# Performance work log

Measured on AMD Instinct MI355X. Metric: run time of the kernel, lower is better.

## Reference

```python
import jax, jax.numpy as jnp
import numpy as np

LN_EPS = 1e-5
LEAKY_SLOPE = 0.01


def setup_inputs() -> dict:
    key = jax.random.key(0)
    k1, k2, k3 = jax.random.split(key, 3)
    n, d, ns = 200000, 512, 1024
    x = jax.random.normal(k1, (n, d), dtype=jnp.float32)
    # Kaiming-ish scale for the projection weight [3d, d]
    W = jax.random.normal(k2, (3 * d, d), dtype=jnp.float32) * (1.0 / np.sqrt(3 * d))
    b = jnp.zeros((d,), dtype=jnp.float32)
    gamma = jnp.ones((d,), dtype=jnp.float32)
    beta = jnp.zeros((d,), dtype=jnp.float32)
    batch = jnp.sort(jax.random.randint(k3, (n,), 0, ns, dtype=jnp.int32))
    return {"x": x, "W": W, "b": b, "gamma": gamma, "beta": beta,
            "batch": batch, "num_segments": ns}


def _pool_mean_max_std(x, batch, num_segments):
    # single-pass style segment reductions: sum, sum-of-squares, count, max
    n = x.shape[0]
    count = jax.ops.segment_sum(jnp.ones((n,), x.dtype), batch, num_segments)  # [S]
    s = jax.ops.segment_sum(x, batch, num_segments)                            # [S,d]
    sq = jax.ops.segment_sum(x * x, batch, num_segments)                       # [S,d]
    cnt = jnp.maximum(count, 1.0)[:, None]
    mean = s / cnt                                                             # global_mean_pool
    # masked dense amax == segment max; empty segments -> finfo.min (NEG fill)
    NEG = jnp.finfo(x.dtype).min
    xmax = jax.ops.segment_max(x, batch, num_segments)
    xmax = jnp.where(jnp.isfinite(xmax), xmax, NEG)
    # scatter_std, unbiased=True, divisor clamped to >= 1 (torch_scatter semantics)
    var = (sq - mean * s) / jnp.maximum(count - 1.0, 1.0)[:, None]
    var = jnp.maximum(var, 0.0)
    safe = jnp.where(var > 0, var, 1.0)
    std = jnp.where(var > 0, jnp.sqrt(safe), 0.0)
    return jnp.concatenate([mean, xmax, std], axis=-1)  # [S, 3d]


def reference(x, W, b, gamma, beta, batch, num_segments):
    pooled = _pool_mean_max_std(x, batch, num_segments)        # [S, 3d]
    h = pooled @ W + b                                          # Linear
    mu = jnp.mean(h, axis=-1, keepdims=True)                    # LayerNorm (eps=1e-5)
    v = jnp.mean((h - mu) ** 2, axis=-1, keepdims=True)
    h = (h - mu) / jnp.sqrt(v + LN_EPS) * gamma + beta
    return jnp.where(h >= 0, h, LEAKY_SLOPE * h)                # LeakyReLU
```

## Files before the change

### kernel.cpp

```cpp
#include <hip/hip_runtime.h>
#include <math.h>

#define D 512
#define K3D 1536
#define NEGF (-3.40282346638528859812e+38f)

__device__ __forceinline__ int lower_bound_dev(const int* __restrict__ b, int n, int v) {
    int lo = 0, hi = n;
    while (lo < hi) {
        int mid = (lo + hi) >> 1;
        if (b[mid] < v) lo = mid + 1; else hi = mid;
    }
    return lo;
}

__device__ __forceinline__ void acc4(float4& s, float4& q, float4& m, const float4 v) {
    s.x += v.x; s.y += v.y; s.z += v.z; s.w += v.w;
    q.x = fmaf(v.x, v.x, q.x); q.y = fmaf(v.y, v.y, q.y);
    q.z = fmaf(v.z, v.z, q.z); q.w = fmaf(v.w, v.w, q.w);
    m.x = fmaxf(m.x, v.x); m.y = fmaxf(m.y, v.y);
    m.z = fmaxf(m.z, v.z); m.w = fmaxf(m.w, v.w);
}

__global__ __launch_bounds__(128) void pool_kernel(
    const float* __restrict__ x, const int* __restrict__ batch,
    float* __restrict__ pooled, int n) {
    const int s = blockIdx.x;
    const int tid = threadIdx.x;
    const int start = lower_bound_dev(batch, n, s);
    const int end   = lower_bound_dev(batch, n, s + 1);

    const float4* __restrict__ xv = (const float4*)x;

    float4 sum = {0.f, 0.f, 0.f, 0.f};
    float4 sq  = {0.f, 0.f, 0.f, 0.f};
    float4 mx  = {-INFINITY, -INFINITY, -INFINITY, -INFINITY};

    int i = start;
    for (; i + 4 <= end; i += 4) {
        float4 v0 = xv[(size_t)(i + 0) * 128 + tid];
        float4 v1 = xv[(size_t)(i + 1) * 128 + tid];
        float4 v2 = xv[(size_t)(i + 2) * 128 + tid];
        float4 v3 = xv[(size_t)(i + 3) * 128 + tid];
        acc4(sum, sq, mx, v0);
        acc4(sum, sq, mx, v1);
        acc4(sum, sq, mx, v2);
        acc4(sum, sq, mx, v3);
    }
    for (; i < end; ++i) {
        float4 v0 = xv[(size_t)i * 128 + tid];
        acc4(sum, sq, mx, v0);
    }

    const float cnt  = (float)(end - start);
    const float inv  = 1.f / fmaxf(cnt, 1.f);
    const float dinv = 1.f / fmaxf(cnt - 1.f, 1.f);

    float4 mean, stdv, mxo;
    mean.x = sum.x * inv; mean.y = sum.y * inv; mean.z = sum.z * inv; mean.w = sum.w * inv;

    float vx = (sq.x - mean.x * sum.x) * dinv;
    float vy = (sq.y - mean.y * sum.y) * dinv;
    float vz = (sq.z - mean.z * sum.z) * dinv;
    float vw = (sq.w - mean.w * sum.w) * dinv;
    vx = fmaxf(vx, 0.f); vy = fmaxf(vy, 0.f); vz = fmaxf(vz, 0.f); vw = fmaxf(vw, 0.f);
    stdv.x = vx > 0.f ? sqrtf(vx) : 0.f;
    stdv.y = vy > 0.f ? sqrtf(vy) : 0.f;
    stdv.z = vz > 0.f ? sqrtf(vz) : 0.f;
    stdv.w = vw > 0.f ? sqrtf(vw) : 0.f;

    mxo.x = isfinite(mx.x) ? mx.x : NEGF;
    mxo.y = isfinite(mx.y) ? mx.y : NEGF;
    mxo.z = isfinite(mx.z) ? mx.z : NEGF;
    mxo.w = isfinite(mx.w) ? mx.w : NEGF;

    float4* prow = (float4*)(pooled + (size_t)s * K3D);
    prow[tid]       = mean;
    prow[128 + tid] = mxo;
    prow[256 + tid] = stdv;
}

#define BM 32
#define BN 64
#define BK 32
#define LDA 36

__global__ __launch_bounds__(128) void gemm_kernel(
    const float* __restrict__ A, const float* __restrict__ W,
    const float* __restrict__ bias, float* __restrict__ H) {
    __shared__ __align__(16) float AsT[BK * LDA];
    __shared__ __align__(16) float Bs[BK * BN];

    const int tid = threadIdx.x;
    const int m0 = blockIdx.y * BM;
    const int j0 = blockIdx.x * BN;
    const int tr = tid >> 4;
    const int tc = tid & 15;

    const int kq = tid & 7;
    const int am = tid >> 3;
    const int jq = tid & 15;
    const int kr = tid >> 4;

    float acc[4][4] = {};

    for (int k0 = 0; k0 < K3D; k0 += BK) {
        float4 a0 = *(const float4*)&A[(size_t)(m0 + am)      * K3D + k0 + 4 * kq];
        float4 a1 = *(const float4*)&A[(size_t)(m0 + am + 16) * K3D + k0 + 4 * kq];
        float4 b0 = *(const float4*)&W[(size_t)(k0 + kr)      * D + j0 + 4 * jq];
        float4 b1 = *(const float4*)&W[(size_t)(k0 + kr +  8) * D + j0 + 4 * jq];
        float4 b2 = *(const float4*)&W[(size_t)(k0 + kr + 16) * D + j0 + 4 * jq];
        float4 b3 = *(const float4*)&W[(size_t)(k0 + kr + 24) * D + j0 + 4 * jq];

        __syncthreads();
        AsT[(4 * kq + 0) * LDA + am] = a0.x;
        AsT[(4 * kq + 1) * LDA + am] = a0.y;
        AsT[(4 * kq + 2) * LDA + am] = a0.z;
        AsT[(4 * kq + 3) * LDA + am] = a0.w;
        AsT[(4 * kq + 0) * LDA + am + 16] = a1.x;
        AsT[(4 * kq + 1) * LDA + am + 16] = a1.y;
        AsT[(4 * kq + 2) * LDA + am + 16] = a1.z;
        AsT[(4 * kq + 3) * LDA + am + 16] = a1.w;
        *(float4*)&Bs[(kr)      * BN + 4 * jq] = b0;
        *(float4*)&Bs[(kr +  8) * BN + 4 * jq] = b1;
        *(float4*)&Bs[(kr + 16) * BN + 4 * jq] = b2;
        *(float4*)&Bs[(kr + 24) * BN + 4 * jq] = b3;
        __syncthreads();

#pragma unroll
        for (int kk = 0; kk < BK; ++kk) {
            float4 av = *(const float4*)&AsT[kk * LDA + 4 * tr];
            float4 bv = *(const float4*)&Bs[kk * BN + 4 * tc];
            acc[0][0] = fmaf(av.x, bv.x, acc[0][0]);
            acc[0][1] = fmaf(av.x, bv.y, acc[0][1]);
            acc[0][2] = fmaf(av.x, bv.z, acc[0][2]);
            acc[0][3] = fmaf(av.x, bv.w, acc[0][3]);
            acc[1][0] = fmaf(av.y, bv.x, acc[1][0]);
            acc[1][1] = fmaf(av.y, bv.y, acc[1][1]);
            acc[1][2] = fmaf(av.y, bv.z, acc[1][2]);
            acc[1][3] = fmaf(av.y, bv.w, acc[1][3]);
            acc[2][0] = fmaf(av.z, bv.x, acc[2][0]);
            acc[2][1] = fmaf(av.z, bv.y, acc[2][1]);
            acc[2][2] = fmaf(av.z, bv.z, acc[2][2]);
            acc[2][3] = fmaf(av.z, bv.w, acc[2][3]);
            acc[3][0] = fmaf(av.w, bv.x, acc[3][0]);
            acc[3][1] = fmaf(av.w, bv.y, acc[3][1]);
            acc[3][2] = fmaf(av.w, bv.z, acc[3][2]);
            acc[3][3] = fmaf(av.w, bv.w, acc[3][3]);
        }
    }

    const float4 bb = *(const float4*)&bias[j0 + 4 * tc];
#pragma unroll
    for (int i = 0; i < 4; ++i) {
        float4 o;
        o.x = acc[i][0] + bb.x;
        o.y = acc[i][1] + bb.y;
        o.z = acc[i][2] + bb.z;
        o.w = acc[i][3] + bb.w;
        *(float4*)&H[(size_t)(m0 + 4 * tr + i) * D + j0 + 4 * tc] = o;
    }
}

__global__ __launch_bounds__(128) void ln_kernel(
    const float* __restrict__ H, const float* __restrict__ gamma,
    const float* __restrict__ beta, float* __restrict__ out) {
    const int row = blockIdx.x;
    const int tid = threadIdx.x;
    float4 v = *(const float4*)&H[(size_t)row * D + 4 * tid];

    float s = v.x + v.y + v.z + v.w;
    float q = v.x * v.x + v.y * v.y + v.z * v.z + v.w * v.w;
#pragma unroll
    for (int off = 32; off > 0; off >>= 1) {
        s += __shfl_down(s, off);
        q += __shfl_down(q, off);
    }
    __shared__ float ls[2], lq[2];
    const int wave = tid >> 6, lane = tid & 63;
    if (lane == 0) { ls[wave] = s; lq[wave] = q; }
    __syncthreads();
    s = ls[0] + ls[1];
    q = lq[0] + lq[1];

    const float mu = s * (1.f / 512.f);
    float var = q * (1.f / 512.f) - mu * mu;
    var = fmaxf(var, 0.f);
    const float r = rsqrtf(var + 1e-5f);

    float4 g  = *(const float4*)&gamma[4 * tid];
    float4 bt = *(const float4*)&beta[4 * tid];
    float4 o;
    o.x = (v.x - mu) * r * g.x + bt.x;
    o.y = (v.y - mu) * r * g.y + bt.y;
    o.z = (v.z - mu) * r * g.z + bt.z;
    o.w = (v.w - mu) * r * g.w + bt.w;
    o.x = o.x >= 0.f ? o.x : 0.01f * o.x;
    o.y = o.y >= 0.f ? o.y : 0.01f * o.y;
    o.z = o.z >= 0.f ? o.z : 0.01f * o.z;
    o.w = o.w >= 0.f ? o.w : 0.01f * o.w;
    *(float4*)&out[(size_t)row * D + 4 * tid] = o;
}

extern "C" void kernel_launch(void* const* d_in, const int* in_sizes, int n_in,
                              void* d_out, int out_size, void* d_ws, size_t ws_size,
                              hipStream_t stream) {
    const float* x     = (const float*)d_in[0];
    const float* W     = (const float*)d_in[1];
    const float* b     = (const float*)d_in[2];
    const float* gamma = (const float*)d_in[3];
    const float* beta  = (const float*)d_in[4];
    const int*   batch = (const int*)d_in[5];
    const int n = in_sizes[5];
    const int S = out_size / D;

    float* pooled = (float*)d_ws;
    float* H      = pooled + (size_t)S * K3D;
    float* out    = (float*)d_out;

    pool_kernel<<<S, 128, 0, stream>>>(x, batch, pooled, n);
    dim3 g2(D / BN, S / BM);
    gemm_kernel<<<g2, 128, 0, stream>>>(pooled, W, b, H);
    ln_kernel<<<S, 128, 0, stream>>>(H, gamma, beta, out);
}
```

Baseline: 625.2 us.

## Use two row-groups per pool block and split-K GEMM with reduction in LayerNorm

The pool kernel now runs 256 threads per segment, with two row-interleaved groups whose partial sum, sum-of-squares and max are combined through shared memory. The GEMM is split along K into four chunks, which multiplies the grid from 256 blocks to 1024 and fills more of the GPU. Each chunk writes its own partial output, and the LayerNorm kernel adds the four partials plus the bias. This costs extra workspace, more global traffic for the partials, and a small change in floating-point summation order.

```diff
diff --git a/kernel.cpp b/kernel.cpp
--- a/kernel.cpp
+++ b/kernel.cpp
@@ -22,11 +22,12 @@
     m.z = fmaxf(m.z, v.z); m.w = fmaxf(m.w, v.w);
 }
 
-__global__ __launch_bounds__(128) void pool_kernel(
+__global__ __launch_bounds__(256) void pool_kernel(
     const float* __restrict__ x, const int* __restrict__ batch,
     float* __restrict__ pooled, int n) {
-    const int s = blockIdx.x;
-    const int tid = threadIdx.x;
+    const int s   = blockIdx.x;
+    const int col = threadIdx.x & 127;
+    const int rw  = threadIdx.x >> 7;
     const int start = lower_bound_dev(batch, n, s);
     const int end   = lower_bound_dev(batch, n, s + 1);
 
@@ -36,64 +37,84 @@
     float4 sq  = {0.f, 0.f, 0.f, 0.f};
     float4 mx  = {-INFINITY, -INFINITY, -INFINITY, -INFINITY};
 
-    int i = start;
-    for (; i + 4 <= end; i += 4) {
-        float4 v0 = xv[(size_t)(i + 0) * 128 + tid];
-        float4 v1 = xv[(size_t)(i + 1) * 128 + tid];
-        float4 v2 = xv[(size_t)(i + 2) * 128 + tid];
-        float4 v3 = xv[(size_t)(i + 3) * 128 + tid];
+    int i = start + rw;
+    for (; i + 6 < end; i += 8) {
+        float4 v0 = xv[(size_t)(i + 0) * 128 + col];
+        float4 v1 = xv[(size_t)(i + 2) * 128 + col];
+        float4 v2 = xv[(size_t)(i + 4) * 128 + col];
+        float4 v3 = xv[(size_t)(i + 6) * 128 + col];
         acc4(sum, sq, mx, v0);
         acc4(sum, sq, mx, v1);
         acc4(sum, sq, mx, v2);
         acc4(sum, sq, mx, v3);
     }
-    for (; i < end; ++i) {
-        float4 v0 = xv[(size_t)i * 128 + tid];
+    for (; i < end; i += 2) {
+        float4 v0 = xv[(size_t)i * 128 + col];
         acc4(sum, sq, mx, v0);
     }
 
-    const float cnt  = (float)(end - start);
-    const float inv  = 1.f / fmaxf(cnt, 1.f);
-    const float dinv = 1.f / fmaxf(cnt - 1.f, 1.f);
-
-    float4 mean, stdv, mxo;
-    mean.x = sum.x * inv; mean.y = sum.y * inv; mean.z = sum.z * inv; mean.w = sum.w * inv;
-
-    float vx = (sq.x - mean.x * sum.x) * dinv;
-    float vy = (sq.y - mean.y * sum.y) * dinv;
-    float vz = (sq.z - mean.z * sum.z) * dinv;
-    float vw = (sq.w - mean.w * sum.w) * dinv;
-    vx = fmaxf(vx, 0.f); vy = fmaxf(vy, 0.f); vz = fmaxf(vz, 0.f); vw = fmaxf(vw, 0.f);
-    stdv.x = vx > 0.f ? sqrtf(vx) : 0.f;
-    stdv.y = vy > 0.f ? sqrtf(vy) : 0.f;
-    stdv.z = vz > 0.f ? sqrtf(vz) : 0.f;
-    stdv.w = vw > 0.f ? sqrtf(vw) : 0.f;
-
-    mxo.x = isfinite(mx.x) ? mx.x : NEGF;
-    mxo.y = isfinite(mx.y) ? mx.y : NEGF;
-    mxo.z = isfinite(mx.z) ? mx.z : NEGF;
-    mxo.w = isfinite(mx.w) ? mx.w : NEGF;
-
-    float4* prow = (float4*)(pooled + (size_t)s * K3D);
-    prow[tid]       = mean;
-    prow[128 + tid] = mxo;
-    prow[256 + tid] = stdv;
+    __shared__ __align__(16) float4 red[3 * 128];
+    if (rw == 1) {
+        red[col]       = sum;
+        red[128 + col] = sq;
+        red[256 + col] = mx;
+    }
+    __syncthreads();
+    if (rw == 0) {
+        float4 s2 = red[col], q2 = red[128 + col], m2 = red[256 + col];
+        sum.x += s2.x; sum.y += s2.y; sum.z += s2.z; sum.w += s2.w;
+        sq.x  += q2.x; sq.y  += q2.y; sq.z  += q2.z; sq.w  += q2.w;
+        mx.x = fmaxf(mx.x, m2.x); mx.y = fmaxf(mx.y, m2.y);
+        mx.z = fmaxf(mx.z, m2.z); mx.w = fmaxf(mx.w, m2.w);
+
+        const float cnt  = (float)(end - start);
+        const float inv  = 1.f / fmaxf(cnt, 1.f);
+        const float dinv = 1.f / fmaxf(cnt - 1.f, 1.f);
+
+        float4 mean, stdv, mxo;
+        mean.x = sum.x * inv; mean.y = sum.y * inv;
+        mean.z = sum.z * inv; mean.w = sum.w * inv;
+
+        float vx = (sq.x - mean.x * sum.x) * dinv;
+        float vy = (sq.y - mean.y * sum.y) * dinv;
+        float vz = (sq.z - mean.z * sum.z) * dinv;
+        float vw = (sq.w - mean.w * sum.w) * dinv;
+        vx = fmaxf(vx, 0.f); vy = fmaxf(vy, 0.f);
+        vz = fmaxf(vz, 0.f); vw = fmaxf(vw, 0.f);
+        stdv.x = vx > 0.f ? sqrtf(vx) : 0.f;
+        stdv.y = vy > 0.f ? sqrtf(vy) : 0.f;
+        stdv.z = vz > 0.f ? sqrtf(vz) : 0.f;
+        stdv.w = vw > 0.f ? sqrtf(vw) : 0.f;
+
+        mxo.x = isfinite(mx.x) ? mx.x : NEGF;
+        mxo.y = isfinite(mx.y) ? mx.y : NEGF;
+        mxo.z = isfinite(mx.z) ? mx.z : NEGF;
+        mxo.w = isfinite(mx.w) ? mx.w : NEGF;
+
+        float4* prow = (float4*)(pooled + (size_t)s * K3D);
+        prow[col]       = mean;
+        prow[128 + col] = mxo;
+        prow[256 + col] = stdv;
+    }
 }
 
 #define BM 32
 #define BN 64
 #define BK 32
 #define LDA 36
+#define SPLITK 4
+#define KCHUNK (K3D / SPLITK)
 
 __global__ __launch_bounds__(128) void gemm_kernel(
     const float* __restrict__ A, const float* __restrict__ W,
-    const float* __restrict__ bias, float* __restrict__ H) {
+    float* __restrict__ Hp, int S) {
     __shared__ __align__(16) float AsT[BK * LDA];
     __shared__ __align__(16) float Bs[BK * BN];
 
     const int tid = threadIdx.x;
     const int m0 = blockIdx.y * BM;
     const int j0 = blockIdx.x * BN;
+    const int kb = blockIdx.z * KCHUNK;
     const int tr = tid >> 4;
     const int tc = tid & 15;
 
@@ -104,7 +125,7 @@
 
     float acc[4][4] = {};
 
-    for (int k0 = 0; k0 < K3D; k0 += BK) {
+    for (int k0 = kb; k0 < kb + KCHUNK; k0 += BK) {
         float4 a0 = *(const float4*)&A[(size_t)(m0 + am)      * K3D + k0 + 4 * kq];
         float4 a1 = *(const float4*)&A[(size_t)(m0 + am + 16) * K3D + k0 + 4 * kq];
         float4 b0 = *(const float4*)&W[(size_t)(k0 + kr)      * D + j0 + 4 * jq];
@@ -150,24 +171,34 @@
         }
     }
 
-    const float4 bb = *(const float4*)&bias[j0 + 4 * tc];
+    float* out = Hp + (size_t)blockIdx.z * S * D;
 #pragma unroll
     for (int i = 0; i < 4; ++i) {
-        float4 o;
-        o.x = acc[i][0] + bb.x;
-        o.y = acc[i][1] + bb.y;
-        o.z = acc[i][2] + bb.z;
-        o.w = acc[i][3] + bb.w;
-        *(float4*)&H[(size_t)(m0 + 4 * tr + i) * D + j0 + 4 * tc] = o;
+        float4 o = {acc[i][0], acc[i][1], acc[i][2], acc[i][3]};
+        *(float4*)&out[(size_t)(m0 + 4 * tr + i) * D + j0 + 4 * tc] = o;
     }
 }
 
 __global__ __launch_bounds__(128) void ln_kernel(
-    const float* __restrict__ H, const float* __restrict__ gamma,
-    const float* __restrict__ beta, float* __restrict__ out) {
+    const float* __restrict__ Hp, const float* __restrict__ bias,
+    const float* __restrict__ gamma, const float* __restrict__ beta,
+    float* __restrict__ out, int S) {
     const int row = blockIdx.x;
     const int tid = threadIdx.x;
-    float4 v = *(const float4*)&H[(size_t)row * D + 4 * tid];
+    const size_t idx = (size_t)row * 128 + tid;
+    const size_t stride = (size_t)S * 128;
+
+    const float4* hp = (const float4*)Hp;
+    float4 v0 = hp[idx];
+    float4 v1 = hp[idx + stride];
+    float4 v2 = hp[idx + 2 * stride];
+    float4 v3 = hp[idx + 3 * stride];
+    float4 bb = *(const float4*)&bias[4 * tid];
+    float4 v;
+    v.x = v0.x + v1.x + v2.x + v3.x + bb.x;
+    v.y = v0.y + v1.y + v2.y + v3.y + bb.y;
+    v.z = v0.z + v1.z + v2.z + v3.z + bb.z;
+    v.w = v0.w + v1.w + v2.w + v3.w + bb.w;
 
     float s = v.x + v.y + v.z + v.w;
     float q = v.x * v.x + v.y * v.y + v.z * v.z + v.w * v.w;
@@ -215,11 +246,11 @@
     const int S = out_size / D;
 
     float* pooled = (float*)d_ws;
-    float* H      = pooled + (size_t)S * K3D;
+    float* Hp     = pooled + (size_t)S * K3D;
     float* out    = (float*)d_out;
 
-    pool_kernel<<<S, 128, 0, stream>>>(x, batch, pooled, n);
-    dim3 g2(D / BN, S / BM);
-    gemm_kernel<<<g2, 128, 0, stream>>>(pooled, W, b, H);
-    ln_kernel<<<S, 128, 0, stream>>>(H, gamma, beta, out);
-}
+    pool_kernel<<<S, 256, 0, stream>>>(x, batch, pooled, n);
+    dim3 g2(D / BN, S / BM, SPLITK);
+    gemm_kernel<<<g2, 128, 0, stream>>>(pooled, W, Hp, S);
+    ln_kernel<<<S, 128, 0, stream>>>(Hp, b, gamma, beta, out, S);
+}
```

New measurement: 583.1 us. 6.7% less time.
